# Optimization experiments

Measured on AMD Instinct MI355X. Metric: run time of the kernel, lower is better.

## Reference

```python
import jax, jax.numpy as jnp
import numpy as np

SPATIAL_SHAPES = [(80, 80), (40, 40), (20, 20)]
NUM_POINTS = [4, 4, 4]
N_HEADS = 8
OFFSET_SCALE = 0.5
LN_EPS = 1e-5


def layer_norm(x, w, b):
    m = x.mean(-1, keepdims=True)
    v = ((x - m) ** 2).mean(-1, keepdims=True)
    return (x - m) * jax.lax.rsqrt(v + LN_EPS) * w + b


def grid_sample(img, grid):
    """Bilinear, zero padding, align_corners=False.
    img: [N, C, H, W], grid: [N, Q, P, 2] in [-1, 1] -> [N, C, Q, P]."""
    N, C, H, W = img.shape
    gx = (grid[..., 0] + 1.0) * (W * 0.5) - 0.5
    gy = (grid[..., 1] + 1.0) * (H * 0.5) - 0.5
    x0 = jnp.floor(gx)
    y0 = jnp.floor(gy)
    wx1 = gx - x0
    wy1 = gy - y0
    x0i = x0.astype(jnp.int32)
    y0i = y0.astype(jnp.int32)
    flat = img.reshape(N, C, H * W)
    Q, P = grid.shape[1], grid.shape[2]

    def corner(xi, yi, w):
        valid = (xi >= 0) & (xi < W) & (yi >= 0) & (yi < H)
        idx = jnp.clip(yi, 0, H - 1) * W + jnp.clip(xi, 0, W - 1)
        v = jnp.take_along_axis(flat, idx.reshape(N, 1, Q * P), axis=2)
        v = v.reshape(N, C, Q, P)
        return v * (w * valid.astype(w.dtype))[:, None]

    return (corner(x0i, y0i, (1 - wx1) * (1 - wy1))
            + corner(x0i + 1, y0i, wx1 * (1 - wy1))
            + corner(x0i, y0i + 1, (1 - wx1) * wy1)
            + corner(x0i + 1, y0i + 1, wx1 * wy1))


def setup_inputs() -> dict:
    key = jax.random.key(0)
    ks = iter(jax.random.split(key, 40))
    B, Q, D, FF = 32, 300, 256, 1024
    S = sum(h * w for h, w in SPATIAL_SHAPES)  # 8400
    SP = sum(NUM_POINTS)  # 12

    def w(shape, scale=0.02):
        return jax.random.normal(next(ks), shape, jnp.float32) * scale

    inp = {
        'hidden_states': jax.random.normal(next(ks), (B, Q, D), jnp.float32),
        'position_embeddings': jax.random.normal(next(ks), (B, Q, D), jnp.float32),
        'reference_points': jax.random.uniform(next(ks), (B, Q, 1, 4), jnp.float32),
        'encoder_hidden_states': jax.random.normal(next(ks), (B, S, D), jnp.float32),
        'q_w': w((D, D)), 'q_b': jnp.zeros((D,), jnp.float32),
        'k_w': w((D, D)), 'k_b': jnp.zeros((D,), jnp.float32),
        'v_w': w((D, D)), 'v_b': jnp.zeros((D,), jnp.float32),
        'o_w': w((D, D)), 'o_b': jnp.zeros((D,), jnp.float32),
        'sa_ln_w': jnp.ones((D,), jnp.float32), 'sa_ln_b': jnp.zeros((D,), jnp.float32),
        'off_w': w((D, N_HEADS * SP * 2)), 'off_b': w((N_HEADS * SP * 2,), 0.1),
        'aw_w': w((D, N_HEADS * SP)), 'aw_b': jnp.zeros((N_HEADS * SP,), jnp.float32),
        'gate_w': w((2 * D, 2 * D)), 'gate_b': jnp.zeros((2 * D,), jnp.float32),
        'gate_ln_w': jnp.ones((D,), jnp.float32), 'gate_ln_b': jnp.zeros((D,), jnp.float32),
        'fc1_w': w((D, FF)), 'fc1_b': jnp.zeros((FF,), jnp.float32),
        'fc2_w': w((FF, D)), 'fc2_b': jnp.zeros((D,), jnp.float32),
        'fin_ln_w': jnp.ones((D,), jnp.float32), 'fin_ln_b': jnp.zeros((D,), jnp.float32),
    }
    return inp


def reference(hidden_states, position_embeddings, reference_points, encoder_hidden_states,
              q_w, q_b, k_w, k_b, v_w, v_b, o_w, o_b, sa_ln_w, sa_ln_b,
              off_w, off_b, aw_w, aw_b, gate_w, gate_b, gate_ln_w, gate_ln_b,
              fc1_w, fc1_b, fc2_w, fc2_b, fin_ln_w, fin_ln_b):
    B, Q, D = hidden_states.shape
    H = N_HEADS
    hd = D // H
    scaling = hd ** -0.5

    # ---- self attention (queries attend to queries, pos added to q/k only) ----
    hq = hidden_states + position_embeddings
    q = ((hq @ q_w + q_b) * scaling).reshape(B, Q, H, hd)
    k = (hq @ k_w + k_b).reshape(B, Q, H, hd)
    v = (hidden_states @ v_w + v_b).reshape(B, Q, H, hd)
    attn = jax.nn.softmax(jnp.einsum('bqhd,bkhd->bhqk', q, k), axis=-1)
    sa = jnp.einsum('bhqk,bkhd->bqhd', attn, v).reshape(B, Q, D) @ o_w + o_b
    hidden_states = layer_norm(hidden_states + sa, sa_ln_w, sa_ln_b)
    second_residual = hidden_states

    # ---- multi-scale deformable cross attention ----
    S = encoder_hidden_states.shape[1]
    SP = sum(NUM_POINTS)
    value = encoder_hidden_states.reshape(B, S, H, hd)
    offs = (hidden_states @ off_w + off_b).reshape(B, Q, H, SP, 2)
    aw = jax.nn.softmax((hidden_states @ aw_w + aw_b).reshape(B, Q, H, SP), axis=-1)
    nps = jnp.asarray([1.0 / n for n in NUM_POINTS for _ in range(n)], hidden_states.dtype)
    offset = offs * nps[:, None] * reference_points[:, :, None, :, 2:] * OFFSET_SCALE
    loc = reference_points[:, :, None, :, :2] + offset          # [B,Q,H,SP,2]
    grids = (2.0 * loc - 1.0).transpose(0, 2, 1, 3, 4).reshape(B * H, Q, SP, 2)
    val = value.transpose(0, 2, 3, 1).reshape(B * H, hd, S)

    sampled = []
    s0, p0 = 0, 0
    for (hl, wl), pl in zip(SPATIAL_SHAPES, NUM_POINTS):
        v_l = val[:, :, s0:s0 + hl * wl].reshape(B * H, hd, hl, wl)
        sampled.append(grid_sample(v_l, grids[:, :, p0:p0 + pl]))
        s0 += hl * wl
        p0 += pl
    sampled = jnp.concatenate(sampled, axis=-1)                 # [B*H,hd,Q,SP]
    aw = aw.transpose(0, 2, 1, 3).reshape(B * H, 1, Q, SP)
    ca = (sampled * aw).sum(-1).reshape(B, D, Q).transpose(0, 2, 1)

    # ---- gated residual ----
    gates = jax.nn.sigmoid(jnp.concatenate([second_residual, ca], -1) @ gate_w + gate_b)
    g1, g2 = gates[..., :D], gates[..., D:]
    hidden_states = layer_norm(g1 * second_residual + g2 * ca, gate_ln_w, gate_ln_b)

    # ---- FFN ----
    ffn = jax.nn.relu(hidden_states @ fc1_w + fc1_b) @ fc2_w + fc2_b
    return layer_norm(hidden_states + ffn, fin_ln_w, fin_ln_b)
```

## Files before the change

kernel.cpp:

```cpp
#include <hip/hip_runtime.h>
#include <cmath>

#define BQ 300
#define DIM 256
#define NH 8
#define HD 32
#define NB 32
#define MROWS 9600
#define SENC 8400

typedef unsigned short ushort_t;
typedef __attribute__((ext_vector_type(8))) short short8;
typedef __attribute__((ext_vector_type(4))) float f32x4;
typedef __attribute__((ext_vector_type(4))) unsigned short us4;
typedef __attribute__((address_space(1))) unsigned int ga_u32;
typedef __attribute__((address_space(3))) unsigned int ls_u32;

__device__ __forceinline__ float bf2f(ushort_t u) {
    union { unsigned u32; float f; } x; x.u32 = ((unsigned)u) << 16; return x.f;
}
__device__ __forceinline__ ushort_t f2bf(float f) {
    union { float f; unsigned u; } x; x.f = f;
    unsigned u = x.u;
    u += 0x7fffu + ((u >> 16) & 1u);
    return (ushort_t)(u >> 16);
}

__global__ __launch_bounds__(256)
void prep_all(const float* __restrict__ hidden, const float* __restrict__ pos,
              ushort_t* __restrict__ hq, ushort_t* __restrict__ hid,
              const float* __restrict__ q_w, const float* __restrict__ k_w,
              const float* __restrict__ v_w, const float* __restrict__ o_w,
              const float* __restrict__ off_w, const float* __restrict__ aw_w,
              const float* __restrict__ gate_w, const float* __restrict__ fc1_w,
              const float* __restrict__ fc2_w,
              ushort_t* __restrict__ qkvT, ushort_t* __restrict__ oT,
              ushort_t* __restrict__ offawT, ushort_t* __restrict__ gT,
              ushort_t* __restrict__ f1T, ushort_t* __restrict__ f2T,
              const float* __restrict__ q_b, const float* __restrict__ k_b,
              const float* __restrict__ v_b, float* __restrict__ qkvb,
              float scal)
{
    const int tid = threadIdx.x;
    if (blockIdx.x < 2400) {
        int i = blockIdx.x * 256 + tid;
        float4 a = ((const float4*)hidden)[i];
        float4 b = ((const float4*)pos)[i];
        us4 uq, uh;
        uq.x = f2bf(a.x + b.x); uq.y = f2bf(a.y + b.y);
        uq.z = f2bf(a.z + b.z); uq.w = f2bf(a.w + b.w);
        uh.x = f2bf(a.x); uh.y = f2bf(a.y); uh.z = f2bf(a.z); uh.w = f2bf(a.w);
        *(us4*)&hq[(size_t)i * 4] = uq;
        *(us4*)&hid[(size_t)i * 4] = uh;
        return;
    }
    __shared__ float t[32][33];
    const int bid = blockIdx.x - 2400;
    const float* src; ushort_t* dst; int K, N, local; float scale = 1.0f;

    if (bid < 64)       { src = q_w;   dst = qkvT;             K = 256; N = 256;  local = bid;       scale = scal; }
    else if (bid < 128) { src = k_w;   dst = qkvT + 256 * 256; K = 256; N = 256;  local = bid - 64; }
    else if (bid < 192) { src = v_w;   dst = qkvT + 512 * 256; K = 256; N = 256;  local = bid - 128; }
    else if (bid < 256) { src = o_w;   dst = oT;               K = 256; N = 256;  local = bid - 192; }
    else if (bid < 304) { src = off_w; dst = offawT;           K = 256; N = 192;  local = bid - 256; }
    else if (bid < 328) { src = aw_w;  dst = offawT + 192 * 256; K = 256; N = 96; local = bid - 304; }
    else if (bid < 336) {
        int l = bid - 328;
        ushort_t* d2 = offawT + 288 * 256 + l * 32;
        for (int e = tid; e < 32 * 32; e += 256) { int r = e >> 5, c = e & 31; d2[r * 256 + c] = 0; }
        return;
    }
    else if (bid < 592) { src = gate_w; dst = gT;  K = 512;  N = 512;  local = bid - 336; }
    else if (bid < 848) { src = fc1_w;  dst = f1T; K = 256;  N = 1024; local = bid - 592; }
    else if (bid < 1104){ src = fc2_w;  dst = f2T; K = 1024; N = 256;  local = bid - 848; }
    else {
        #pragma unroll
        for (int j = 0; j < 3; ++j) {
            int c = j * 256 + tid;
            float v = (j == 0) ? q_b[tid] * scal : (j == 1) ? k_b[tid] : v_b[tid];
            qkvb[c] = v;
        }
        return;
    }
    const int tilesx = N >> 5;
    const int n0 = (local % tilesx) * 32, k0 = (local / tilesx) * 32;
    const int tx = tid & 31, ty = tid >> 5;
    #pragma unroll
    for (int i = 0; i < 4; ++i)
        t[ty + i * 8][tx] = src[(size_t)(k0 + ty + i * 8) * N + n0 + tx];
    __syncthreads();
    #pragma unroll
    for (int i = 0; i < 4; ++i)
        dst[(size_t)(n0 + ty + i * 8) * K + k0 + tx] = f2bf(t[tx][ty + i * 8] * scale);
}

template<int BM, int BN, int ACT, bool OBF>
__global__ __launch_bounds__(256)
void gemm_mfma(const ushort_t* __restrict__ A1, const ushort_t* __restrict__ A2,
               int asplit, int lda,
               const ushort_t* __restrict__ Bt, int K,
               const float* __restrict__ bias, const float* __restrict__ bias2,
               int bsplit, int N,
               float* __restrict__ Cf, ushort_t* __restrict__ Cb, int ldc)
{
    __shared__ ushort_t As[BM * 32];
    __shared__ ushort_t Bs[BN * 32];
    const int tid = threadIdx.x;
    const int row0 = blockIdx.y * BM, col0 = blockIdx.x * BN;
    const ushort_t* __restrict__ A = (col0 < asplit) ? A1 : A2;
    const int lane = tid & 63, wid = tid >> 6;
    const int wm = wid >> 1, wn = wid & 1;
    constexpr int FM = BM / 32, FN = BN / 32;
    const int r16 = lane & 15, kg = lane >> 4;
    const int rsub = lane >> 2, c8 = (lane & 3) * 8;

    f32x4 acc[FM][FN];
    #pragma unroll
    for (int m = 0; m < FM; ++m)
        #pragma unroll
        for (int n = 0; n < FN; ++n) {
            f32x4 z = {0.f, 0.f, 0.f, 0.f};
            acc[m][n] = z;
        }

    for (int k0 = 0; k0 < K; k0 += 32) {
        #pragma unroll
        for (int i = wid; i < BM / 16; i += 4) {
            const int r = i * 16 + rsub;
            __builtin_amdgcn_global_load_lds(
                (const ga_u32*)(const void*)&A[(size_t)(row0 + r) * lda + k0 + c8],
                (ls_u32*)(void*)&As[i * 512], 16, 0, 0);
        }
        #pragma unroll
        for (int i = wid; i < BN / 16; i += 4) {
            const int r = i * 16 + rsub;
            __builtin_amdgcn_global_load_lds(
                (const ga_u32*)(const void*)&Bt[(size_t)(col0 + r) * K + k0 + c8],
                (ls_u32*)(void*)&Bs[i * 512], 16, 0, 0);
        }
        __syncthreads();
        short8 a[FM], b[FN];
        #pragma unroll
        for (int m = 0; m < FM; ++m)
            a[m] = *(const short8*)&As[(wm * (BM / 2) + m * 16 + r16) * 32 + kg * 8];
        #pragma unroll
        for (int n = 0; n < FN; ++n)
            b[n] = *(const short8*)&Bs[(wn * (BN / 2) + n * 16 + r16) * 32 + kg * 8];
        #pragma unroll
        for (int m = 0; m < FM; ++m)
            #pragma unroll
            for (int n = 0; n < FN; ++n)
                acc[m][n] = __builtin_amdgcn_mfma_f32_16x16x32_bf16(a[m], b[n], acc[m][n], 0, 0, 0);
        __syncthreads();
    }

    #pragma unroll
    for (int m = 0; m < FM; ++m) {
        #pragma unroll
        for (int n = 0; n < FN; ++n) {
            int colb = col0 + wn * (BN / 2) + n * 16 + r16;
            float bs;
            if (colb < bsplit) bs = bias[colb];
            else if (colb < N) bs = bias2[colb - bsplit];
            else bs = 0.0f;
            #pragma unroll
            for (int r = 0; r < 4; ++r) {
                int row = row0 + wm * (BM / 2) + m * 16 + kg * 4 + r;
                float v = acc[m][n][r] + bs;
                if (ACT == 1) v = fmaxf(v, 0.0f);
                if (ACT == 2) v = 1.0f / (1.0f + __expf(-v));
                if (OBF) Cb[(size_t)row * ldc + colb] = f2bf(v);
                else     Cf[(size_t)row * ldc + colb] = v;
            }
        }
    }
}

__global__ __launch_bounds__(256)
void gemm_ln(const ushort_t* __restrict__ A, int lda,
             const ushort_t* __restrict__ Bt, int K,
             const float* __restrict__ gb, const float* __restrict__ Y,
             const float* __restrict__ lnw, const float* __restrict__ lnb,
             float* __restrict__ outf, ushort_t* __restrict__ outbf, int ldout)
{
    constexpr int LDT = 40;
    __shared__ ushort_t As[32 * LDT];
    __shared__ ushort_t Bs[256 * LDT];
    __shared__ float sred[2][32], qred[2][32];
    const int tid = threadIdx.x;
    const int row0 = blockIdx.x * 32;
    const int lane = tid & 63, wid = tid >> 6;
    const int wm = wid >> 1, wn = wid & 1;
    const int r16 = lane & 15, kg = lane >> 4;

    f32x4 acc[8];
    #pragma unroll
    for (int n = 0; n < 8; ++n) { f32x4 z = {0.f,0.f,0.f,0.f}; acc[n] = z; }

    for (int k0 = 0; k0 < K; k0 += 32) {
        if (tid < 128) {
            int r = tid >> 2, cc = tid & 3;
            *(short8*)&As[r * LDT + cc * 8] =
                *(const short8*)&A[(size_t)(row0 + r) * lda + k0 + cc * 8];
        }
        #pragma unroll
        for (int c = 0; c < 4; ++c) {
            int idx = tid + c * 256;
            int r = idx >> 2, cc = idx & 3;
            *(short8*)&Bs[r * LDT + cc * 8] =
                *(const short8*)&Bt[(size_t)r * K + k0 + cc * 8];
        }
        __syncthreads();
        short8 a = *(const short8*)&As[(wm * 16 + r16) * LDT + kg * 8];
        #pragma unroll
        for (int n = 0; n < 8; ++n) {
            short8 b = *(const short8*)&Bs[(wn * 128 + n * 16 + r16) * LDT + kg * 8];
            acc[n] = __builtin_amdgcn_mfma_f32_16x16x32_bf16(a, b, acc[n], 0, 0, 0);
        }
        __syncthreads();
    }

    float s[4] = {0.f, 0.f, 0.f, 0.f}, q[4] = {0.f, 0.f, 0.f, 0.f};
    #pragma unroll
    for (int n = 0; n < 8; ++n) {
        const int col = wn * 128 + n * 16 + r16;
        const float gbv = gb[col];
        #pragma unroll
        for (int r = 0; r < 4; ++r) {
            const int row = row0 + wm * 16 + kg * 4 + r;
            float t = acc[n][r] + gbv + Y[(size_t)row * 256 + col];
            acc[n][r] = t;
            s[r] += t; q[r] += t * t;
        }
    }
    #pragma unroll
    for (int off = 1; off < 16; off <<= 1) {
        #pragma unroll
        for (int r = 0; r < 4; ++r) {
            s[r] += __shfl_xor(s[r], off);
            q[r] += __shfl_xor(q[r], off);
        }
    }
    if (r16 == 0) {
        #pragma unroll
        for (int r = 0; r < 4; ++r) {
            sred[wn][wm * 16 + kg * 4 + r] = s[r];
            qred[wn][wm * 16 + kg * 4 + r] = q[r];
        }
    }
    __syncthreads();
    float mn[4], inv[4];
    #pragma unroll
    for (int r = 0; r < 4; ++r) {
        const int rl = wm * 16 + kg * 4 + r;
        float S = sred[0][rl] + sred[1][rl];
        float Q = qred[0][rl] + qred[1][rl];
        float mean = S * (1.0f / 256.0f);
        float var = Q * (1.0f / 256.0f) - mean * mean;
        mn[r] = mean; inv[r] = rsqrtf(var + 1e-5f);
    }
    #pragma unroll
    for (int n = 0; n < 8; ++n) {
        const int col = wn * 128 + n * 16 + r16;
        const float w = lnw[col], b = lnb[col];
        #pragma unroll
        for (int r = 0; r < 4; ++r) {
            const int row = row0 + wm * 16 + kg * 4 + r;
            float v = (acc[n][r] - mn[r]) * inv[r] * w + b;
            if (outf)  outf[(size_t)row * 256 + col] = v;
            if (outbf) outbf[(size_t)row * ldout + col] = f2bf(v);
        }
    }
}

__global__ __launch_bounds__(256)
void attn_flash(const ushort_t* __restrict__ QKV, ushort_t* __restrict__ O)
{
    __shared__ ushort_t ks[64 * 40];
    __shared__ ushort_t vt[32 * 72];
    __shared__ float    ss[32 * 68];
    __shared__ ushort_t ps[32 * 72];
    __shared__ float    ml[32], ll[32], fl[32];

    const int orig = blockIdx.x;
    const int wg = (orig & 7) * 320 + (orig >> 3);
    const int qc = wg % 10, bh = wg / 10;
    const int b = bh >> 3, h = bh & 7;
    const int q0 = qc * 32;
    const int nq = (BQ - q0 < 32) ? (BQ - q0) : 32;

    const int tid = threadIdx.x;
    const int lane = tid & 63, wid = tid >> 6;
    const int r16 = lane & 15, kg = lane >> 4;
    const int wm = wid >> 1, wn = wid & 1;

    if (tid < 32) { ml[tid] = -1e30f; ll[tid] = 0.f; }

    short8 aq[2];
    #pragma unroll
    for (int rt = 0; rt < 2; ++rt) {
        int qr = q0 + rt * 16 + r16;
        if (qr > BQ - 1) qr = BQ - 1;
        aq[rt] = *(const short8*)&QKV[((size_t)(b * BQ + qr)) * 768 + h * 32 + kg * 8];
    }
    f32x4 oacc = {0.f, 0.f, 0.f, 0.f};

    for (int kt = 0; kt < 5; ++kt) {
        __syncthreads();
        {
            int kk = tid >> 2, c8 = (tid & 3) * 8;
            int ki = kt * 64 + kk;
            short8 kv = {0, 0, 0, 0, 0, 0, 0, 0};
            short8 vv = {0, 0, 0, 0, 0, 0, 0, 0};
            if (ki < BQ) {
                size_t gi = ((size_t)(b * BQ + ki)) * 768 + h * 32 + c8;
                kv = *(const short8*)&QKV[gi + 256];
                vv = *(const short8*)&QKV[gi + 512];
            }
            *(short8*)&ks[kk * 40 + c8] = kv;
            #pragma unroll
            for (int j = 0; j < 8; ++j) vt[(c8 + j) * 72 + kk] = (ushort_t)vv[j];
        }
        __syncthreads();
        {
            short8 bk = *(const short8*)&ks[(wid * 16 + r16) * 40 + kg * 8];
            #pragma unroll
            for (int rt = 0; rt < 2; ++rt) {
                f32x4 sacc = {0.f, 0.f, 0.f, 0.f};
                sacc = __builtin_amdgcn_mfma_f32_16x16x32_bf16(aq[rt], bk, sacc, 0, 0, 0);
                #pragma unroll
                for (int r = 0; r < 4; ++r)
                    ss[(rt * 16 + kg * 4 + r) * 68 + wid * 16 + r16] = sacc[r];
            }
        }
        __syncthreads();
        #pragma unroll
        for (int j = 0; j < 8; ++j) {
            int row = wid * 8 + j;
            float s = ss[row * 68 + lane];
            if (kt * 64 + lane >= BQ) s = -1e30f;
            float tm = s;
            #pragma unroll
            for (int off = 32; off; off >>= 1) tm = fmaxf(tm, __shfl_xor(tm, off));
            float mold = ml[row];
            float mnew = fmaxf(mold, tm);
            float p = __expf(s - mnew);
            float psum = p;
            #pragma unroll
            for (int off = 32; off; off >>= 1) psum += __shfl_xor(psum, off);
            if (lane == 0) {
                float f = __expf(mold - mnew);
                ml[row] = mnew;
                ll[row] = ll[row] * f + psum;
                fl[row] = f;
            }
            ps[row * 72 + lane] = f2bf(p);
        }
        __syncthreads();
        {
            #pragma unroll
            for (int r = 0; r < 4; ++r)
                oacc[r] *= fl[wm * 16 + kg * 4 + r];
            #pragma unroll
            for (int kstep = 0; kstep < 2; ++kstep) {
                short8 pa = *(const short8*)&ps[(wm * 16 + r16) * 72 + kstep * 32 + kg * 8];
                short8 bv = *(const short8*)&vt[(wn * 16 + r16) * 72 + kstep * 32 + kg * 8];
                oacc = __builtin_amdgcn_mfma_f32_16x16x32_bf16(pa, bv, oacc, 0, 0, 0);
            }
        }
    }
    __syncthreads();
    #pragma unroll
    for (int r = 0; r < 4; ++r) {
        int rowl = wm * 16 + kg * 4 + r;
        if (rowl < nq) {
            float v = oacc[r] / ll[rowl];
            O[((size_t)(b * BQ + q0 + rowl)) * 256 + h * 32 + wn * 16 + r16] = f2bf(v);
        }
    }
}

__global__ __launch_bounds__(256)
void ln_gate(const ushort_t* __restrict__ C2, const ushort_t* __restrict__ G,
             const float* __restrict__ w, const float* __restrict__ b,
             float* __restrict__ outf, ushort_t* __restrict__ outbf)
{
    const int row = blockIdx.x * 4 + (threadIdx.x >> 6);
    const int lane = threadIdx.x & 63;
    float v[4];
    #pragma unroll
    for (int i = 0; i < 4; ++i) {
        int c = lane + 64 * i;
        float h1 = bf2f(C2[(size_t)row * 512 + c]);
        float ca = bf2f(C2[(size_t)row * 512 + 256 + c]);
        float g1 = bf2f(G[(size_t)row * 512 + c]);
        float g2 = bf2f(G[(size_t)row * 512 + 256 + c]);
        v[i] = g1 * h1 + g2 * ca;
    }
    float s = v[0] + v[1] + v[2] + v[3];
    float s2 = v[0]*v[0] + v[1]*v[1] + v[2]*v[2] + v[3]*v[3];
    #pragma unroll
    for (int off = 32; off; off >>= 1) { s += __shfl_xor(s, off); s2 += __shfl_xor(s2, off); }
    const float mean = s * (1.0f / DIM);
    const float var = s2 * (1.0f / DIM) - mean * mean;
    const float inv = rsqrtf(var + 1e-5f);
    #pragma unroll
    for (int i = 0; i < 4; ++i) {
        int c = lane + 64 * i;
        float r = (v[i] - mean) * inv * w[c] + b[c];
        outf[(size_t)row * DIM + c] = r;
        outbf[(size_t)row * DIM + c] = f2bf(r);
    }
}

__global__ __launch_bounds__(256)
void sample_kernel(const float* __restrict__ enc, const float* __restrict__ offaw,
                   const float* __restrict__ ref, ushort_t* __restrict__ C2out)
{
    __shared__ float sofs[4][320];
    __shared__ float sref[4][4];

    const int orig = blockIdx.x;
    const int blk = (orig & 7) * 300 + (orig >> 3);
    const int b = blk / 75;
    const int q0 = (blk % 75) * 4;
    const int tid = threadIdx.x;
    const int qq = tid >> 6;
    const int h = (tid >> 3) & 7;
    const int d4 = tid & 7;
    const int bq = b * BQ + q0 + qq;

    for (int e = tid; e < 4 * 80; e += 256) {
        int row = e / 80, c4 = e % 80;
        ((float4*)&sofs[row][0])[c4] =
            ((const float4*)(offaw + (size_t)(b * BQ + q0 + row) * 320))[c4];
    }
    if (tid < 16)
        sref[tid >> 2][tid & 3] = ref[(size_t)(b * BQ + q0 + (tid >> 2)) * 4 + (tid & 3)];
    __syncthreads();

    const float rx = sref[qq][0], ry = sref[qq][1];
    const float rw = sref[qq][2], rh = sref[qq][3];
    const float* op = &sofs[qq][h * 24];
    const float* ap = &sofs[qq][192 + h * 12];

    float wgt[12];
    float mx = -1e30f;
    #pragma unroll
    for (int j = 0; j < 12; ++j) { wgt[j] = ap[j]; mx = fmaxf(mx, wgt[j]); }
    float sum = 0.0f;
    #pragma unroll
    for (int j = 0; j < 12; ++j) { wgt[j] = __expf(wgt[j] - mx); sum += wgt[j]; }
    const float isum = 1.0f / sum;

    f32x4 acc = {0.f, 0.f, 0.f, 0.f};
    int p = 0;
    #pragma unroll
    for (int l = 0; l < 3; ++l) {
        const int Wl = (l == 0) ? 80 : (l == 1 ? 40 : 20);
        const int Hl = Wl;
        const int soff = (l == 0) ? 0 : (l == 1 ? 6400 : 8000);
        const float* base = enc + ((size_t)(b * SENC + soff)) * DIM + h * HD + d4 * 4;
        #pragma unroll
        for (int pp = 0; pp < 4; ++pp, ++p) {
            const float ox = op[p * 2 + 0], oy = op[p * 2 + 1];
            const float lx = rx + ox * 0.25f * rw * 0.5f;
            const float ly = ry + oy * 0.25f * rh * 0.5f;
            const float gx = lx * (float)Wl - 0.5f;
            const float gy = ly * (float)Hl - 0.5f;
            const float x0f = floorf(gx), y0f = floorf(gy);
            const int x0 = (int)x0f, y0 = (int)y0f;
            const float wx1 = gx - x0f, wy1 = gy - y0f;
            const float wx0 = 1.0f - wx1, wy0 = 1.0f - wy1;
            const bool vx0 = (x0 >= 0) & (x0 < Wl);
            const bool vx1 = (x0 + 1 >= 0) & (x0 + 1 < Wl);
            const bool vy0 = (y0 >= 0) & (y0 < Hl);
            const bool vy1 = (y0 + 1 >= 0) & (y0 + 1 < Hl);
            const int xc0 = min(max(x0, 0), Wl - 1);
            const int xc1 = min(max(x0 + 1, 0), Wl - 1);
            const int yc0 = min(max(y0, 0), Hl - 1);
            const int yc1 = min(max(y0 + 1, 0), Hl - 1);
            const float aw2 = wgt[p] * isum;
            const float w00 = wx0 * wy0 * ((vx0 & vy0) ? aw2 : 0.0f);
            const float w10 = wx1 * wy0 * ((vx1 & vy0) ? aw2 : 0.0f);
            const float w01 = wx0 * wy1 * ((vx0 & vy1) ? aw2 : 0.0f);
            const float w11 = wx1 * wy1 * ((vx1 & vy1) ? aw2 : 0.0f);
            f32x4 c00 = *(const f32x4*)&base[((size_t)(yc0 * Wl + xc0)) * DIM];
            f32x4 c10 = *(const f32x4*)&base[((size_t)(yc0 * Wl + xc1)) * DIM];
            f32x4 c01 = *(const f32x4*)&base[((size_t)(yc1 * Wl + xc0)) * DIM];
            f32x4 c11 = *(const f32x4*)&base[((size_t)(yc1 * Wl + xc1)) * DIM];
            #pragma unroll
            for (int r = 0; r < 4; ++r)
                acc[r] += w00 * c00[r] + w10 * c10[r] + w01 * c01[r] + w11 * c11[r];
        }
    }
    us4 u;
    u.x = f2bf(acc[0]); u.y = f2bf(acc[1]); u.z = f2bf(acc[2]); u.w = f2bf(acc[3]);
    *(us4*)&C2out[(size_t)bq * 512 + 256 + h * HD + d4 * 4] = u;
}

extern "C" void kernel_launch(void* const* d_in, const int* in_sizes, int n_in,
                              void* d_out, int out_size, void* d_ws, size_t ws_size,
                              hipStream_t stream)
{
    (void)in_sizes; (void)n_in; (void)out_size; (void)ws_size;
    const float* hidden   = (const float*)d_in[0];
    const float* pos      = (const float*)d_in[1];
    const float* ref      = (const float*)d_in[2];
    const float* enc      = (const float*)d_in[3];
    const float* q_w      = (const float*)d_in[4];
    const float* q_b      = (const float*)d_in[5];
    const float* k_w      = (const float*)d_in[6];
    const float* k_b      = (const float*)d_in[7];
    const float* v_w      = (const float*)d_in[8];
    const float* v_b      = (const float*)d_in[9];
    const float* o_w      = (const float*)d_in[10];
    const float* o_b      = (const float*)d_in[11];
    const float* sa_ln_w  = (const float*)d_in[12];
    const float* sa_ln_b  = (const float*)d_in[13];
    const float* off_w    = (const float*)d_in[14];
    const float* off_b    = (const float*)d_in[15];
    const float* aw_w     = (const float*)d_in[16];
    const float* aw_b     = (const float*)d_in[17];
    const float* gate_w   = (const float*)d_in[18];
    const float* gate_b   = (const float*)d_in[19];
    const float* gate_ln_w= (const float*)d_in[20];
    const float* gate_ln_b= (const float*)d_in[21];
    const float* fc1_w    = (const float*)d_in[22];
    const float* fc1_b    = (const float*)d_in[23];
    const float* fc2_w    = (const float*)d_in[24];
    const float* fc2_b    = (const float*)d_in[25];
    const float* fin_ln_w = (const float*)d_in[26];
    const float* fin_ln_b = (const float*)d_in[27];
    float* out = (float*)d_out;

    char* wsb = (char*)d_ws;
    ushort_t* hqbf   = (ushort_t*)(wsb + 0);
    ushort_t* hidbf  = (ushort_t*)(wsb + 4915200);
    ushort_t* QKV    = (ushort_t*)(wsb + 9830400);
    ushort_t* aobf   = (ushort_t*)(wsb + 24576000);
    ushort_t* C2     = (ushort_t*)(wsb + 9830400);
    float*    offaw  = (float*)(wsb + 19660800);
    ushort_t* gatesbf= (ushort_t*)(wsb + 0);
    ushort_t* midbf  = (ushort_t*)(wsb + 19660800);
    ushort_t* h2bf   = (ushort_t*)(wsb + 39321600);
    ushort_t* qkvT   = (ushort_t*)(wsb + 44236800);
    ushort_t* oT     = (ushort_t*)(wsb + 44630016);
    ushort_t* offawT = (ushort_t*)(wsb + 44761088);
    ushort_t* gT     = (ushort_t*)(wsb + 44924928);
    ushort_t* f1T    = (ushort_t*)(wsb + 45449216);
    ushort_t* f2T    = (ushort_t*)(wsb + 45973504);
    float*    qkvb   = (float*)(wsb + 46497792);

    const dim3 blk(256);
    const float scal = 0.17677669529663687f;
    const int BIG = 1 << 30;

    prep_all<<<dim3(3505), blk, 0, stream>>>(hidden, pos, hqbf, hidbf,
                                             q_w, k_w, v_w, o_w, off_w, aw_w,
                                             gate_w, fc1_w, fc2_w,
                                             qkvT, oT, offawT, gT, f1T, f2T,
                                             q_b, k_b, v_b, qkvb, scal);

    gemm_mfma<64,128,0,true><<<dim3(6,150), blk, 0, stream>>>(hqbf, hidbf, 512, 256, qkvT, 256, qkvb, nullptr, 768, 768, nullptr, QKV, 768);

    attn_flash<<<dim3(2560), blk, 0, stream>>>(QKV, aobf);

    gemm_ln<<<dim3(300), blk, 0, stream>>>(aobf, 256, oT, 256, o_b, hidden,
                                           sa_ln_w, sa_ln_b, nullptr, C2, 512);

    gemm_mfma<64,64,0,false><<<dim3(5,150), blk, 0, stream>>>(C2, nullptr, BIG, 512, offawT, 256, off_b, aw_b, 192, 288, offaw, nullptr, 320);

    sample_kernel<<<dim3(2400), blk, 0, stream>>>(enc, offaw, ref, C2);

    gemm_mfma<64,128,2,true><<<dim3(4,150), blk, 0, stream>>>(C2, nullptr, BIG, 512, gT, 512, gate_b, nullptr, 512, 512, nullptr, gatesbf, 512);
    ln_gate<<<dim3(2400), blk, 0, stream>>>(C2, gatesbf, gate_ln_w, gate_ln_b, out, h2bf);

    gemm_mfma<128,128,1,true><<<dim3(8,75), blk, 0, stream>>>(h2bf, nullptr, BIG, 256, f1T, 256, fc1_b, nullptr, 1024, 1024, nullptr, midbf, 1024);
    gemm_ln<<<dim3(300), blk, 0, stream>>>(midbf, 1024, f2T, 1024, fc2_b, out,
                                           fin_ln_w, fin_ln_b, out, nullptr, 0);
}
```

Measured before the change: 238.3 us.

## Fuse gate GEMM, sigmoid and gated-residual LayerNorm into one kernel

Replaces the separate gate GEMM (sigmoid epilogue, bf16 gates written to workspace) and the ln_gate kernel with one kernel. Each block computes all 512 gate columns for 16 rows, keeps the gates in shared memory, then applies the gated residual and LayerNorm. This removes one launch and the round trip of the gates tensor through global memory. In exchange, each block re-streams the whole 512x512 gate weight for only 16 rows, a single MFMA tile per k-step, with no double buffering and only 600 blocks, so weight traffic is higher and the GEMM itself may run less efficiently.

New measurement: 246.6 us. 1.04x slower.

```diff
diff --git a/kernel.cpp b/kernel.cpp
--- a/kernel.cpp
+++ b/kernel.cpp
@@ -274,6 +274,94 @@
 }
 
 __global__ __launch_bounds__(256)
+void gemm_gate_ln(const ushort_t* __restrict__ C2, const ushort_t* __restrict__ Bt,
+                  const float* __restrict__ gb,
+                  const float* __restrict__ lnw, const float* __restrict__ lnb,
+                  float* __restrict__ outf, ushort_t* __restrict__ outbf)
+{
+    __shared__ ushort_t As[16 * 32];
+    __shared__ ushort_t Bs[512 * 32];
+    const int tid = threadIdx.x;
+    const int row0 = blockIdx.x * 16;
+    const int lane = tid & 63, wid = tid >> 6;
+    const int r16 = lane & 15, kg = lane >> 4;
+    const int rsub = lane >> 2, c8 = (lane & 3) * 8;
+
+    f32x4 acc[8];
+    #pragma unroll
+    for (int n = 0; n < 8; ++n) { f32x4 z = {0.f,0.f,0.f,0.f}; acc[n] = z; }
+
+    for (int k0 = 0; k0 < 512; k0 += 32) {
+        if (wid == 0) {
+            __builtin_amdgcn_global_load_lds(
+                (const ga_u32*)(const void*)&C2[(size_t)(row0 + rsub) * 512 + k0 + c8],
+                (ls_u32*)(void*)&As[0], 16, 0, 0);
+        }
+        #pragma unroll
+        for (int i = wid; i < 32; i += 4) {
+            const int r = i * 16 + rsub;
+            __builtin_amdgcn_global_load_lds(
+                (const ga_u32*)(const void*)&Bt[(size_t)r * 512 + k0 + c8],
+                (ls_u32*)(void*)&Bs[i * 512], 16, 0, 0);
+        }
+        __syncthreads();
+        short8 a = *(const short8*)&As[r16 * 32 + kg * 8];
+        #pragma unroll
+        for (int n = 0; n < 8; ++n) {
+            short8 b = *(const short8*)&Bs[(wid * 128 + n * 16 + r16) * 32 + kg * 8];
+            acc[n] = __builtin_amdgcn_mfma_f32_16x16x32_bf16(a, b, acc[n], 0, 0, 0);
+        }
+        __syncthreads();
+    }
+
+    ushort_t* gates = (ushort_t*)Bs;
+    #pragma unroll
+    for (int n = 0; n < 8; ++n) {
+        const int col = wid * 128 + n * 16 + r16;
+        const float gbv = gb[col];
+        #pragma unroll
+        for (int r = 0; r < 4; ++r) {
+            const int row_l = kg * 4 + r;
+            float g = 1.0f / (1.0f + __expf(-(acc[n][r] + gbv)));
+            gates[row_l * 512 + col] = f2bf(g);
+        }
+    }
+    __syncthreads();
+
+    for (int j = 0; j < 4; ++j) {
+        const int row_l = wid * 4 + j;
+        const int row = row0 + row_l;
+        us4 h14 = *(const us4*)&C2[(size_t)row * 512 + lane * 4];
+        us4 ca4 = *(const us4*)&C2[(size_t)row * 512 + 256 + lane * 4];
+        us4 g14 = *(const us4*)&gates[row_l * 512 + lane * 4];
+        us4 g24 = *(const us4*)&gates[row_l * 512 + 256 + lane * 4];
+        float v[4];
+        float s = 0.f, s2 = 0.f;
+        #pragma unroll
+        for (int i = 0; i < 4; ++i) {
+            v[i] = bf2f(g14[i]) * bf2f(h14[i]) + bf2f(g24[i]) * bf2f(ca4[i]);
+            s += v[i]; s2 += v[i] * v[i];
+        }
+        #pragma unroll
+        for (int off = 32; off; off >>= 1) {
+            s += __shfl_xor(s, off); s2 += __shfl_xor(s2, off);
+        }
+        const float mean = s * (1.0f / 256.0f);
+        const float var = s2 * (1.0f / 256.0f) - mean * mean;
+        const float inv = rsqrtf(var + 1e-5f);
+        f32x4 rf; us4 rb;
+        #pragma unroll
+        for (int i = 0; i < 4; ++i) {
+            const int c = lane * 4 + i;
+            float r = (v[i] - mean) * inv * lnw[c] + lnb[c];
+            rf[i] = r; rb[i] = f2bf(r);
+        }
+        *(f32x4*)&outf[(size_t)row * 256 + lane * 4] = rf;
+        *(us4*)&outbf[(size_t)row * 256 + lane * 4] = rb;
+    }
+}
+
+__global__ __launch_bounds__(256)
 void attn_flash(const ushort_t* __restrict__ QKV, ushort_t* __restrict__ O)
 {
     __shared__ ushort_t ks[64 * 40];
@@ -377,39 +465,6 @@
             float v = oacc[r] / ll[rowl];
             O[((size_t)(b * BQ + q0 + rowl)) * 256 + h * 32 + wn * 16 + r16] = f2bf(v);
         }
-    }
-}
-
-__global__ __launch_bounds__(256)
-void ln_gate(const ushort_t* __restrict__ C2, const ushort_t* __restrict__ G,
-             const float* __restrict__ w, const float* __restrict__ b,
-             float* __restrict__ outf, ushort_t* __restrict__ outbf)
-{
-    const int row = blockIdx.x * 4 + (threadIdx.x >> 6);
-    const int lane = threadIdx.x & 63;
-    float v[4];
-    #pragma unroll
-    for (int i = 0; i < 4; ++i) {
-        int c = lane + 64 * i;
-        float h1 = bf2f(C2[(size_t)row * 512 + c]);
-        float ca = bf2f(C2[(size_t)row * 512 + 256 + c]);
-        float g1 = bf2f(G[(size_t)row * 512 + c]);
-        float g2 = bf2f(G[(size_t)row * 512 + 256 + c]);
-        v[i] = g1 * h1 + g2 * ca;
-    }
-    float s = v[0] + v[1] + v[2] + v[3];
-    float s2 = v[0]*v[0] + v[1]*v[1] + v[2]*v[2] + v[3]*v[3];
-    #pragma unroll
-    for (int off = 32; off; off >>= 1) { s += __shfl_xor(s, off); s2 += __shfl_xor(s2, off); }
-    const float mean = s * (1.0f / DIM);
-    const float var = s2 * (1.0f / DIM) - mean * mean;
-    const float inv = rsqrtf(var + 1e-5f);
-    #pragma unroll
-    for (int i = 0; i < 4; ++i) {
-        int c = lane + 64 * i;
-        float r = (v[i] - mean) * inv * w[c] + b[c];
-        outf[(size_t)row * DIM + c] = r;
-        outbf[(size_t)row * DIM + c] = f2bf(r);
     }
 }
 
@@ -541,7 +596,6 @@
     ushort_t* aobf   = (ushort_t*)(wsb + 24576000);
     ushort_t* C2     = (ushort_t*)(wsb + 9830400);
     float*    offaw  = (float*)(wsb + 19660800);
-    ushort_t* gatesbf= (ushort_t*)(wsb + 0);
     ushort_t* midbf  = (ushort_t*)(wsb + 19660800);
     ushort_t* h2bf   = (ushort_t*)(wsb + 39321600);
     ushort_t* qkvT   = (ushort_t*)(wsb + 44236800);
@@ -573,8 +627,7 @@
 
     sample_kernel<<<dim3(2400), blk, 0, stream>>>(enc, offaw, ref, C2);
 
-    gemm_mfma<64,128,2,true><<<dim3(4,150), blk, 0, stream>>>(C2, nullptr, BIG, 512, gT, 512, gate_b, nullptr, 512, 512, nullptr, gatesbf, 512);
-    ln_gate<<<dim3(2400), blk, 0, stream>>>(C2, gatesbf, gate_ln_w, gate_ln_b, out, h2bf);
+    gemm_gate_ln<<<dim3(600), blk, 0, stream>>>(C2, gT, gate_b, gate_ln_w, gate_ln_b, out, h2bf);
 
     gemm_mfma<128,128,1,true><<<dim3(8,75), blk, 0, stream>>>(h2bf, nullptr, BIG, 256, f1T, 256, fc1_b, nullptr, 1024, 1024, nullptr, midbf, 1024);
     gemm_ln<<<dim3(300), blk, 0, stream>>>(midbf, 1024, f2T, 1024, fc2_b, out,
```
